# Kernel tuning notes

Measured on AMD Instinct MI355X. Metric: run time of the kernel, lower is better.

Reference implementation:

```python
import jax, jax.numpy as jnp
import numpy as np

E, H, I, T, K = 32, 1024, 768, 2048, 8


def setup_inputs() -> dict:
    key = jax.random.key(0)
    ks = jax.random.split(key, 6)
    hidden_states = jax.random.normal(ks[0], (T, H), dtype=jnp.float32)
    routing_weights = jax.random.uniform(ks[1], (T, K), dtype=jnp.float32)
    selected_experts = jax.random.randint(ks[2], (T, K), 0, E, dtype=jnp.int32)
    scale = 0.02
    gate_proj = jax.random.normal(ks[3], (E, I, H), dtype=jnp.float32) * scale
    up_proj = jax.random.normal(ks[4], (E, I, H), dtype=jnp.float32) * scale
    down_proj = jax.random.normal(ks[5], (E, H, I), dtype=jnp.float32) * scale
    return {
        "hidden_states": hidden_states,
        "routing_weights": routing_weights,
        "selected_experts": selected_experts,
        "gate_proj": gate_proj,
        "up_proj": up_proj,
        "down_proj": down_proj,
    }


def reference(hidden_states, routing_weights, selected_experts, gate_proj, up_proj, down_proj):
    # hidden_states: [T, H]; routing_weights/selected_experts: [T, K]
    # gate/up: [E, I, H]; down: [E, H, I]
    T_, _ = hidden_states.shape
    E_ = gate_proj.shape[0]
    # combine[t, e] = sum_k routing_weights[t, k] * 1[selected_experts[t, k] == e]
    combine = jnp.zeros((T_, E_), hidden_states.dtype).at[
        jnp.arange(T_)[:, None], selected_experts
    ].add(routing_weights)
    g = jnp.einsum('th,eih->eti', hidden_states, gate_proj)   # [E, T, I]
    u = jnp.einsum('th,eih->eti', hidden_states, up_proj)     # [E, T, I]
    h = jax.nn.silu(g) * u                                    # SwiGLU
    d = jnp.einsum('eti,ehi->eth', h, down_proj)              # [E, T, H]
    out = jnp.einsum('eth,te->th', d, combine)                # weighted combine
    return out
```

## Files before the change

### kernel.cpp

```cpp
#include <hip/hip_runtime.h>
#include <hip/hip_bf16.h>
#include <math.h>

#define E_N 32
#define H_N 1024
#define I_N 768
#define T_N 2048
#define K_N 8
#define MT  128
#define NPAIRS (T_N * K_N)
#define MAX_SLOTS (NPAIRS + E_N * MT)
#define MAX_TILES (NPAIRS / MT + E_N)

typedef __attribute__((ext_vector_type(8))) short bf16x8;
typedef __attribute__((ext_vector_type(4))) short bf16x4;
typedef __attribute__((ext_vector_type(8))) float f32x8;
typedef __attribute__((ext_vector_type(4))) float f32x4;

__device__ __forceinline__ unsigned pk2(float a, float b) {
    unsigned ua = __float_as_uint(a) + 0x8000u;
    unsigned ub = __float_as_uint(b) + 0x8000u;
    return (ua >> 16) | (ub & 0xffff0000u);
}
__device__ __forceinline__ bf16x8 cvt8(f32x8 v) {
    union { unsigned u[4]; bf16x8 h; } r;
    r.u[0] = pk2(v[0], v[1]); r.u[1] = pk2(v[2], v[3]);
    r.u[2] = pk2(v[4], v[5]); r.u[3] = pk2(v[6], v[7]);
    return r.h;
}
__device__ __forceinline__ float bf2f(short s) {
    return __uint_as_float(((unsigned)(unsigned short)s) << 16);
}

__device__ __forceinline__ void gload16(const void* g, void* l) {
    __builtin_amdgcn_global_load_lds(
        (const __attribute__((address_space(1))) unsigned int*)g,
        (__attribute__((address_space(3))) unsigned int*)l, 16, 0, 0);
}

__global__ void route_kernel(const int* __restrict__ sel,
                             int* __restrict__ slot_token,
                             int* __restrict__ pair_slot,
                             int* __restrict__ tile_expert,
                             int* __restrict__ tile_row0,
                             int* __restrict__ n_tiles_out) {
    __shared__ int cnt[E_N], off[E_N], cur[E_N];
    int tid = threadIdx.x;
    if (tid < E_N) cnt[tid] = 0;
    __syncthreads();
    for (int p = tid; p < NPAIRS; p += blockDim.x)
        atomicAdd(&cnt[sel[p]], 1);
    __syncthreads();
    if (tid == 0) {
        int acc = 0, tt = 0;
        for (int e = 0; e < E_N; ++e) {
            off[e] = acc;
            cur[e] = 0;
            int nt = (cnt[e] + MT - 1) / MT;
            for (int i = 0; i < nt; ++i) {
                tile_expert[tt] = e;
                tile_row0[tt] = acc + i * MT;
                ++tt;
            }
            acc += nt * MT;
        }
        *n_tiles_out = tt;
    }
    __syncthreads();
    for (int p = tid; p < NPAIRS; p += blockDim.x) {
        int e = sel[p];
        int slot = off[e] + atomicAdd(&cur[e], 1);
        slot_token[slot] = p / K_N;
        pair_slot[p] = slot;
    }
}

__global__ __launch_bounds__(256) void gather_kernel(
    const float* __restrict__ hs,
    const int* __restrict__ slot_token,
    short* __restrict__ x_buf) {
    int idx = blockIdx.x * 256 + threadIdx.x;
    int slot = idx >> 8;
    int pos = (idx & 255) * 4;
    int tok = slot_token[slot];
    union { unsigned u[2]; bf16x4 s; } o;
    if (tok >= 0) {
        f32x4 v = *(const f32x4*)(hs + (size_t)tok * H_N + pos);
        o.u[0] = pk2(v[0], v[1]);
        o.u[1] = pk2(v[2], v[3]);
    } else {
        o.u[0] = 0; o.u[1] = 0;
    }
    *(bf16x4*)(x_buf + (size_t)slot * H_N + pos) = o.s;
}

__global__ __launch_bounds__(256) void cvt_kernel(
    const float* __restrict__ src, short* __restrict__ dst, int n8) {
    int i = blockIdx.x * 256 + threadIdx.x;
    int stride = gridDim.x * 256;
    for (; i < n8; i += stride) {
        f32x8 v = *(const f32x8*)(src + (size_t)i * 8);
        *(bf16x8*)(dst + (size_t)i * 8) = cvt8(v);
    }
}

__global__ __launch_bounds__(256, 2) void gateup_kernel(
    const short* __restrict__ x_buf,
    const short* __restrict__ wg,
    const short* __restrict__ wu,
    const int* __restrict__ tile_expert,
    const int* __restrict__ tile_row0,
    const int* __restrict__ n_tiles,
    __hip_bfloat16* __restrict__ h_buf) {
    int id = blockIdx.x;
    int W = (id & 7) * 120 + (id >> 3);
    int tile = W % MAX_TILES;
    int ycol = W / MAX_TILES;
    if (tile >= *n_tiles) return;
    __shared__ short sA[128 * 32];
    __shared__ short sG[128 * 32];
    __shared__ short sU[128 * 32];
    int e = tile_expert[tile];
    int row0 = tile_row0[tile];
    int col0 = ycol * 128;
    int tid = threadIdx.x;
    int wave = tid >> 6, lane = tid & 63, quad = lane >> 4, r16 = lane & 15;
    int m0w = (wave >> 1) * 64, n0w = (wave & 1) * 64;
    int srow = lane >> 2;
    int scb = (lane & 3) * 8;

    f32x4 accG[4][4], accU[4][4];
#pragma unroll
    for (int i = 0; i < 4; ++i)
#pragma unroll
        for (int j = 0; j < 4; ++j) {
            accG[i][j] = (f32x4){0.f, 0.f, 0.f, 0.f};
            accU[i][j] = (f32x4){0.f, 0.f, 0.f, 0.f};
        }

    const short* Ag = x_buf + (size_t)row0 * H_N;
    const short* Gg = wg + ((size_t)e * I_N + col0) * H_N;
    const short* Ug = wu + ((size_t)e * I_N + col0) * H_N;

#pragma unroll 1
    for (int k0 = 0; k0 < H_N; k0 += 32) {
        __syncthreads();
#pragma unroll
        for (int c = 0; c < 2; ++c) {
            int rb = (wave * 2 + c) * 16;
            size_t goff = (size_t)(rb + srow) * H_N + k0 + scb;
            gload16(Ag + goff, &sA[rb * 32]);
            gload16(Gg + goff, &sG[rb * 32]);
            gload16(Ug + goff, &sU[rb * 32]);
        }
        __syncthreads();
        bf16x8 af[4], bg[4], bu[4];
#pragma unroll
        for (int mi = 0; mi < 4; ++mi)
            af[mi] = *(const bf16x8*)&sA[(m0w + mi * 16 + r16) * 32 + quad * 8];
#pragma unroll
        for (int ni = 0; ni < 4; ++ni) {
            bg[ni] = *(const bf16x8*)&sG[(n0w + ni * 16 + r16) * 32 + quad * 8];
            bu[ni] = *(const bf16x8*)&sU[(n0w + ni * 16 + r16) * 32 + quad * 8];
        }
        __builtin_amdgcn_s_setprio(1);
#pragma unroll
        for (int mi = 0; mi < 4; ++mi)
#pragma unroll
            for (int ni = 0; ni < 4; ++ni) {
                accG[mi][ni] = __builtin_amdgcn_mfma_f32_16x16x32_bf16(af[mi], bg[ni], accG[mi][ni], 0, 0, 0);
                accU[mi][ni] = __builtin_amdgcn_mfma_f32_16x16x32_bf16(af[mi], bu[ni], accU[mi][ni], 0, 0, 0);
            }
        __builtin_amdgcn_s_setprio(0);
    }
#pragma unroll
    for (int mi = 0; mi < 4; ++mi)
#pragma unroll
        for (int ni = 0; ni < 4; ++ni)
#pragma unroll
            for (int r = 0; r < 4; ++r) {
                int m = m0w + mi * 16 + quad * 4 + r;
                int n = col0 + n0w + ni * 16 + r16;
                float g = accG[mi][ni][r], u = accU[mi][ni][r];
                float hval = g * u / (1.0f + __expf(-g));
                h_buf[(size_t)(row0 + m) * I_N + n] = __float2bfloat16(hval);
            }
}

__global__ __launch_bounds__(256, 3) void down_kernel(
    const __hip_bfloat16* __restrict__ h_buf,
    const short* __restrict__ wd,
    const int* __restrict__ tile_expert,
    const int* __restrict__ tile_row0,
    const int* __restrict__ n_tiles,
    short* __restrict__ d_buf) {
    int id = blockIdx.x;
    int W = (id & 7) * 160 + (id >> 3);
    int tile = W % MAX_TILES;
    int ycol = W / MAX_TILES;
    if (tile >= *n_tiles) return;
    __shared__ short sA[128 * 32];
    __shared__ short sB[128 * 32];
    int e = tile_expert[tile];
    int row0 = tile_row0[tile];
    int col0 = ycol * 128;
    int tid = threadIdx.x;
    int wave = tid >> 6, lane = tid & 63, quad = lane >> 4, r16 = lane & 15;
    int m0w = (wave >> 1) * 64, n0w = (wave & 1) * 64;
    int srow = lane >> 2;
    int scb = (lane & 3) * 8;

    f32x4 acc[4][4];
#pragma unroll
    for (int i = 0; i < 4; ++i)
#pragma unroll
        for (int j = 0; j < 4; ++j) acc[i][j] = (f32x4){0.f, 0.f, 0.f, 0.f};

    const short* Ag = (const short*)h_buf + (size_t)row0 * I_N;
    const short* Bg = wd + ((size_t)e * H_N + col0) * I_N;

#pragma unroll 1
    for (int k0 = 0; k0 < I_N; k0 += 32) {
        __syncthreads();
#pragma unroll
        for (int c = 0; c < 2; ++c) {
            int rb = (wave * 2 + c) * 16;
            size_t goff = (size_t)(rb + srow) * I_N + k0 + scb;
            gload16(Ag + goff, &sA[rb * 32]);
            gload16(Bg + goff, &sB[rb * 32]);
        }
        __syncthreads();
        bf16x8 af[4], bf[4];
#pragma unroll
        for (int mi = 0; mi < 4; ++mi)
            af[mi] = *(const bf16x8*)&sA[(m0w + mi * 16 + r16) * 32 + quad * 8];
#pragma unroll
        for (int ni = 0; ni < 4; ++ni)
            bf[ni] = *(const bf16x8*)&sB[(n0w + ni * 16 + r16) * 32 + quad * 8];
        __builtin_amdgcn_s_setprio(1);
#pragma unroll
        for (int mi = 0; mi < 4; ++mi)
#pragma unroll
            for (int ni = 0; ni < 4; ++ni)
                acc[mi][ni] = __builtin_amdgcn_mfma_f32_16x16x32_bf16(af[mi], bf[ni], acc[mi][ni], 0, 0, 0);
        __builtin_amdgcn_s_setprio(0);
    }
#pragma unroll
    for (int mi = 0; mi < 4; ++mi)
#pragma unroll
        for (int ni = 0; ni < 4; ++ni)
#pragma unroll
            for (int r = 0; r < 4; ++r) {
                int m = m0w + mi * 16 + quad * 4 + r;
                int n = col0 + n0w + ni * 16 + r16;
                unsigned u = __float_as_uint(acc[mi][ni][r]) + 0x8000u;
                d_buf[(size_t)(row0 + m) * H_N + n] = (short)(u >> 16);
            }
}

__global__ __launch_bounds__(256) void combine_kernel(
    const short* __restrict__ d_buf,
    const int* __restrict__ pair_slot,
    const float* __restrict__ rw,
    float* __restrict__ out) {
    int idx = blockIdx.x * blockDim.x + threadIdx.x;
    int t = idx >> 10;
    int h = idx & (H_N - 1);
    float acc = 0.f;
#pragma unroll
    for (int k = 0; k < K_N; ++k) {
        int slot = pair_slot[t * K_N + k];
        float w = rw[t * K_N + k];
        acc += w * bf2f(d_buf[(size_t)slot * H_N + h]);
    }
    out[idx] = acc;
}

extern "C" void kernel_launch(void* const* d_in, const int* in_sizes, int n_in,
                              void* d_out, int out_size, void* d_ws, size_t ws_size,
                              hipStream_t stream) {
    const float* hs   = (const float*)d_in[0];
    const float* rw   = (const float*)d_in[1];
    const int*   sel  = (const int*)d_in[2];
    const float* gate = (const float*)d_in[3];
    const float* up   = (const float*)d_in[4];
    const float* down = (const float*)d_in[5];
    float* out = (float*)d_out;

    const size_t WN = (size_t)E_N * I_N * H_N;
    char* ws = (char*)d_ws;
    int* slot_token  = (int*)ws;  ws += ((size_t)MAX_SLOTS * 4 + 255) / 256 * 256;
    int* pair_slot   = (int*)ws;  ws += ((size_t)NPAIRS * 4 + 255) / 256 * 256;
    int* tile_expert = (int*)ws;  ws += ((size_t)MAX_TILES * 4 + 255) / 256 * 256;
    int* tile_row0   = (int*)ws;  ws += ((size_t)MAX_TILES * 4 + 255) / 256 * 256;
    int* n_tiles     = (int*)ws;  ws += 256;
    short* x_buf = (short*)ws;    ws += ((size_t)MAX_SLOTS * H_N * 2 + 255) / 256 * 256;
    __hip_bfloat16* h_buf = (__hip_bfloat16*)ws;
    ws += ((size_t)MAX_SLOTS * I_N * 2 + 255) / 256 * 256;
    short* wg = (short*)ws;
    short* wu = wg + WN;
    short* wd = wg;
    short* d_buf = x_buf;

    hipMemsetAsync(slot_token, 0xFF, (size_t)MAX_SLOTS * 4, stream);
    route_kernel<<<1, 256, 0, stream>>>(sel, slot_token, pair_slot,
                                        tile_expert, tile_row0, n_tiles);
    gather_kernel<<<(MAX_SLOTS * H_N / 4) / 256, 256, 0, stream>>>(hs, slot_token, x_buf);

    const int N8 = (int)(WN / 8);
    cvt_kernel<<<2048, 256, 0, stream>>>(gate, wg, N8);
    cvt_kernel<<<2048, 256, 0, stream>>>(up, wu, N8);

    gateup_kernel<<<MAX_TILES * (I_N / 128), 256, 0, stream>>>(
        x_buf, wg, wu, tile_expert, tile_row0, n_tiles, h_buf);

    cvt_kernel<<<2048, 256, 0, stream>>>(down, wd, N8);

    down_kernel<<<MAX_TILES * (H_N / 128), 256, 0, stream>>>(
        h_buf, wd, tile_expert, tile_row0, n_tiles, d_buf);

    combine_kernel<<<(T_N * H_N) / 256, 256, 0, stream>>>(d_buf, pair_slot,
                                                          rw, out);
}
```

Measured before the change: 524.2 us.

## Parallelize routing, fuse gate/up weight conversion, and double K-step per barrier in GEMMs

Splits the single-block routing kernel into a multi-block histogram, a scan, and a multi-block placement kernel, so routing no longer runs serially on one workgroup. Gate and up weight conversion are fused into one launch. Both GEMM kernels now stage 64-wide K slices (two 32-wide LDS buffers) per barrier pair, halving the number of synchronizations at the cost of doubled LDS use, which may lower occupancy. Slot ordering within an expert now depends on cross-block atomics, so it is nondeterministic.

```diff
diff --git a/kernel.cpp b/kernel.cpp
--- a/kernel.cpp
+++ b/kernel.cpp
@@ -38,25 +38,28 @@
         (__attribute__((address_space(3))) unsigned int*)l, 16, 0, 0);
 }
 
-__global__ void route_kernel(const int* __restrict__ sel,
-                             int* __restrict__ slot_token,
-                             int* __restrict__ pair_slot,
-                             int* __restrict__ tile_expert,
-                             int* __restrict__ tile_row0,
-                             int* __restrict__ n_tiles_out) {
-    __shared__ int cnt[E_N], off[E_N], cur[E_N];
+__global__ __launch_bounds__(256) void hist_kernel(const int* __restrict__ sel,
+                                                   int* __restrict__ cnt_g) {
+    __shared__ int cnt[E_N];
     int tid = threadIdx.x;
     if (tid < E_N) cnt[tid] = 0;
     __syncthreads();
-    for (int p = tid; p < NPAIRS; p += blockDim.x)
-        atomicAdd(&cnt[sel[p]], 1);
+    int p = blockIdx.x * 256 + tid;
+    atomicAdd(&cnt[sel[p]], 1);
     __syncthreads();
-    if (tid == 0) {
+    if (tid < E_N) atomicAdd(&cnt_g[tid], cnt[tid]);
+}
+
+__global__ void scan_kernel(const int* __restrict__ cnt_g,
+                            int* __restrict__ off_g,
+                            int* __restrict__ tile_expert,
+                            int* __restrict__ tile_row0,
+                            int* __restrict__ n_tiles_out) {
+    if (threadIdx.x == 0) {
         int acc = 0, tt = 0;
         for (int e = 0; e < E_N; ++e) {
-            off[e] = acc;
-            cur[e] = 0;
-            int nt = (cnt[e] + MT - 1) / MT;
+            off_g[e] = acc;
+            int nt = (cnt_g[e] + MT - 1) / MT;
             for (int i = 0; i < nt; ++i) {
                 tile_expert[tt] = e;
                 tile_row0[tt] = acc + i * MT;
@@ -66,13 +69,19 @@
         }
         *n_tiles_out = tt;
     }
-    __syncthreads();
-    for (int p = tid; p < NPAIRS; p += blockDim.x) {
-        int e = sel[p];
-        int slot = off[e] + atomicAdd(&cur[e], 1);
-        slot_token[slot] = p / K_N;
-        pair_slot[p] = slot;
-    }
+}
+
+__global__ __launch_bounds__(256) void place_kernel(
+    const int* __restrict__ sel,
+    const int* __restrict__ off_g,
+    int* __restrict__ cur_g,
+    int* __restrict__ slot_token,
+    int* __restrict__ pair_slot) {
+    int p = blockIdx.x * 256 + threadIdx.x;
+    int e = sel[p];
+    int slot = off_g[e] + atomicAdd(&cur_g[e], 1);
+    slot_token[slot] = p / K_N;
+    pair_slot[p] = slot;
 }
 
 __global__ __launch_bounds__(256) void gather_kernel(
@@ -94,6 +103,18 @@
     *(bf16x4*)(x_buf + (size_t)slot * H_N + pos) = o.s;
 }
 
+__global__ __launch_bounds__(256) void cvt2_kernel(
+    const float* __restrict__ s0, short* __restrict__ d0,
+    const float* __restrict__ s1, short* __restrict__ d1, int n8) {
+    int i = blockIdx.x * 256 + threadIdx.x;
+    int stride = gridDim.x * 256;
+    for (; i < n8; i += stride) {
+        f32x8 v0 = *(const f32x8*)(s0 + (size_t)i * 8);
+        *(bf16x8*)(d0 + (size_t)i * 8) = cvt8(v0);
+        f32x8 v1 = *(const f32x8*)(s1 + (size_t)i * 8);
+        *(bf16x8*)(d1 + (size_t)i * 8) = cvt8(v1);
+    }
+}
 __global__ __launch_bounds__(256) void cvt_kernel(
     const float* __restrict__ src, short* __restrict__ dst, int n8) {
     int i = blockIdx.x * 256 + threadIdx.x;
@@ -117,9 +138,9 @@
     int tile = W % MAX_TILES;
     int ycol = W / MAX_TILES;
     if (tile >= *n_tiles) return;
-    __shared__ short sA[128 * 32];
-    __shared__ short sG[128 * 32];
-    __shared__ short sU[128 * 32];
+    __shared__ short sA[2][128 * 32];
+    __shared__ short sG[2][128 * 32];
+    __shared__ short sU[2][128 * 32];
     int e = tile_expert[tile];
     int row0 = tile_row0[tile];
     int col0 = ycol * 128;
@@ -143,35 +164,41 @@
     const short* Ug = wu + ((size_t)e * I_N + col0) * H_N;
 
 #pragma unroll 1
-    for (int k0 = 0; k0 < H_N; k0 += 32) {
+    for (int k0 = 0; k0 < H_N; k0 += 64) {
         __syncthreads();
 #pragma unroll
         for (int c = 0; c < 2; ++c) {
             int rb = (wave * 2 + c) * 16;
             size_t goff = (size_t)(rb + srow) * H_N + k0 + scb;
-            gload16(Ag + goff, &sA[rb * 32]);
-            gload16(Gg + goff, &sG[rb * 32]);
-            gload16(Ug + goff, &sU[rb * 32]);
+            gload16(Ag + goff,      &sA[0][rb * 32]);
+            gload16(Ag + goff + 32, &sA[1][rb * 32]);
+            gload16(Gg + goff,      &sG[0][rb * 32]);
+            gload16(Gg + goff + 32, &sG[1][rb * 32]);
+            gload16(Ug + goff,      &sU[0][rb * 32]);
+            gload16(Ug + goff + 32, &sU[1][rb * 32]);
         }
         __syncthreads();
-        bf16x8 af[4], bg[4], bu[4];
-#pragma unroll
-        for (int mi = 0; mi < 4; ++mi)
-            af[mi] = *(const bf16x8*)&sA[(m0w + mi * 16 + r16) * 32 + quad * 8];
-#pragma unroll
-        for (int ni = 0; ni < 4; ++ni) {
-            bg[ni] = *(const bf16x8*)&sG[(n0w + ni * 16 + r16) * 32 + quad * 8];
-            bu[ni] = *(const bf16x8*)&sU[(n0w + ni * 16 + r16) * 32 + quad * 8];
-        }
-        __builtin_amdgcn_s_setprio(1);
-#pragma unroll
-        for (int mi = 0; mi < 4; ++mi)
+#pragma unroll
+        for (int ks = 0; ks < 2; ++ks) {
+            bf16x8 af[4], bg[4], bu[4];
+#pragma unroll
+            for (int mi = 0; mi < 4; ++mi)
+                af[mi] = *(const bf16x8*)&sA[ks][(m0w + mi * 16 + r16) * 32 + quad * 8];
 #pragma unroll
             for (int ni = 0; ni < 4; ++ni) {
-                accG[mi][ni] = __builtin_amdgcn_mfma_f32_16x16x32_bf16(af[mi], bg[ni], accG[mi][ni], 0, 0, 0);
-                accU[mi][ni] = __builtin_amdgcn_mfma_f32_16x16x32_bf16(af[mi], bu[ni], accU[mi][ni], 0, 0, 0);
+                bg[ni] = *(const bf16x8*)&sG[ks][(n0w + ni * 16 + r16) * 32 + quad * 8];
+                bu[ni] = *(const bf16x8*)&sU[ks][(n0w + ni * 16 + r16) * 32 + quad * 8];
             }
-        __builtin_amdgcn_s_setprio(0);
+            __builtin_amdgcn_s_setprio(1);
+#pragma unroll
+            for (int mi = 0; mi < 4; ++mi)
+#pragma unroll
+                for (int ni = 0; ni < 4; ++ni) {
+                    accG[mi][ni] = __builtin_amdgcn_mfma_f32_16x16x32_bf16(af[mi], bg[ni], accG[mi][ni], 0, 0, 0);
+                    accU[mi][ni] = __builtin_amdgcn_mfma_f32_16x16x32_bf16(af[mi], bu[ni], accU[mi][ni], 0, 0, 0);
+                }
+            __builtin_amdgcn_s_setprio(0);
+        }
     }
 #pragma unroll
     for (int mi = 0; mi < 4; ++mi)
@@ -199,8 +226,8 @@
     int tile = W % MAX_TILES;
     int ycol = W / MAX_TILES;
     if (tile >= *n_tiles) return;
-    __shared__ short sA[128 * 32];
-    __shared__ short sB[128 * 32];
+    __shared__ short sA[2][128 * 32];
+    __shared__ short sB[2][128 * 32];
     int e = tile_expert[tile];
     int row0 = tile_row0[tile];
     int col0 = ycol * 128;
@@ -220,30 +247,35 @@
     const short* Bg = wd + ((size_t)e * H_N + col0) * I_N;
 
 #pragma unroll 1
-    for (int k0 = 0; k0 < I_N; k0 += 32) {
+    for (int k0 = 0; k0 < I_N; k0 += 64) {
         __syncthreads();
 #pragma unroll
         for (int c = 0; c < 2; ++c) {
             int rb = (wave * 2 + c) * 16;
             size_t goff = (size_t)(rb + srow) * I_N + k0 + scb;
-            gload16(Ag + goff, &sA[rb * 32]);
-            gload16(Bg + goff, &sB[rb * 32]);
+            gload16(Ag + goff,      &sA[0][rb * 32]);
+            gload16(Ag + goff + 32, &sA[1][rb * 32]);
+            gload16(Bg + goff,      &sB[0][rb * 32]);
+            gload16(Bg + goff + 32, &sB[1][rb * 32]);
         }
         __syncthreads();
-        bf16x8 af[4], bf[4];
-#pragma unroll
-        for (int mi = 0; mi < 4; ++mi)
-            af[mi] = *(const bf16x8*)&sA[(m0w + mi * 16 + r16) * 32 + quad * 8];
-#pragma unroll
-        for (int ni = 0; ni < 4; ++ni)
-            bf[ni] = *(const bf16x8*)&sB[(n0w + ni * 16 + r16) * 32 + quad * 8];
-        __builtin_amdgcn_s_setprio(1);
-#pragma unroll
-        for (int mi = 0; mi < 4; ++mi)
+#pragma unroll
+        for (int ks = 0; ks < 2; ++ks) {
+            bf16x8 af[4], bf[4];
+#pragma unroll
+            for (int mi = 0; mi < 4; ++mi)
+                af[mi] = *(const bf16x8*)&sA[ks][(m0w + mi * 16 + r16) * 32 + quad * 8];
 #pragma unroll
             for (int ni = 0; ni < 4; ++ni)
-                acc[mi][ni] = __builtin_amdgcn_mfma_f32_16x16x32_bf16(af[mi], bf[ni], acc[mi][ni], 0, 0, 0);
-        __builtin_amdgcn_s_setprio(0);
+                bf[ni] = *(const bf16x8*)&sB[ks][(n0w + ni * 16 + r16) * 32 + quad * 8];
+            __builtin_amdgcn_s_setprio(1);
+#pragma unroll
+            for (int mi = 0; mi < 4; ++mi)
+#pragma unroll
+                for (int ni = 0; ni < 4; ++ni)
+                    acc[mi][ni] = __builtin_amdgcn_mfma_f32_16x16x32_bf16(af[mi], bf[ni], acc[mi][ni], 0, 0, 0);
+            __builtin_amdgcn_s_setprio(0);
+        }
     }
 #pragma unroll
     for (int mi = 0; mi < 4; ++mi)
@@ -294,6 +326,9 @@
     int* tile_expert = (int*)ws;  ws += ((size_t)MAX_TILES * 4 + 255) / 256 * 256;
     int* tile_row0   = (int*)ws;  ws += ((size_t)MAX_TILES * 4 + 255) / 256 * 256;
     int* n_tiles     = (int*)ws;  ws += 256;
+    int* cnt_g       = (int*)ws;  ws += 256;
+    int* cur_g       = (int*)ws;  ws += 256;
+    int* off_g       = (int*)ws;  ws += 256;
     short* x_buf = (short*)ws;    ws += ((size_t)MAX_SLOTS * H_N * 2 + 255) / 256 * 256;
     __hip_bfloat16* h_buf = (__hip_bfloat16*)ws;
     ws += ((size_t)MAX_SLOTS * I_N * 2 + 255) / 256 * 256;
@@ -303,13 +338,16 @@
     short* d_buf = x_buf;
 
     hipMemsetAsync(slot_token, 0xFF, (size_t)MAX_SLOTS * 4, stream);
-    route_kernel<<<1, 256, 0, stream>>>(sel, slot_token, pair_slot,
-                                        tile_expert, tile_row0, n_tiles);
+    hipMemsetAsync(cnt_g, 0, 512, stream);
+
+    hist_kernel<<<NPAIRS / 256, 256, 0, stream>>>(sel, cnt_g);
+    scan_kernel<<<1, 64, 0, stream>>>(cnt_g, off_g, tile_expert, tile_row0, n_tiles);
+    place_kernel<<<NPAIRS / 256, 256, 0, stream>>>(sel, off_g, cur_g,
+                                                   slot_token, pair_slot);
     gather_kernel<<<(MAX_SLOTS * H_N / 4) / 256, 256, 0, stream>>>(hs, slot_token, x_buf);
 
     const int N8 = (int)(WN / 8);
-    cvt_kernel<<<2048, 256, 0, stream>>>(gate, wg, N8);
-    cvt_kernel<<<2048, 256, 0, stream>>>(up, wu, N8);
+    cvt2_kernel<<<2048, 256, 0, stream>>>(gate, wg, up, wu, N8);
 
     gateup_kernel<<<MAX_TILES * (I_N / 128), 256, 0, stream>>>(
         x_buf, wg, wu, tile_expert, tile_row0, n_tiles, h_buf);
```

Measured after the change: 513.0 us. 1.02x faster.
